# Performance work log

Hardware: AMD Instinct MI355X
Metric: run time of the kernel (lower is better)

Reference implementation:

```python
import jax, jax.numpy as jnp
import numpy as np

K_UP = 5
UP = 2
KS = 3
C_IN = 256


def pixel_shuffle(x, r):
    N, C, H, W = x.shape
    x = x.reshape(N, C // (r * r), r, r, H, W)
    return x.transpose(0, 1, 4, 2, 5, 3).reshape(N, C // (r * r), H * r, W * r)


def conv2d(x, w, b, pad):
    y = jax.lax.conv_general_dilated(
        x, w, window_strides=(1, 1), padding=[(pad, pad), (pad, pad)],
        dimension_numbers=('NCHW', 'OIHW', 'NCHW'))
    return y + b[None, :, None, None]


def setup_inputs() -> dict:
    key = jax.random.key(0)
    ks = jax.random.split(key, 7)
    C = C_IN
    Cd = C // 2
    Ce = UP * UP * K_UP * K_UP  # 100
    x = jax.random.normal(ks[0], (4, C, 64, 64), dtype=jnp.float32)
    # kaiming-normal-ish inits, biases small uniform (torch default)
    w_down = jax.random.normal(ks[1], (Cd, C, 1, 1), dtype=jnp.float32) * np.sqrt(2.0 / C)
    b_down = jax.random.uniform(ks[2], (Cd,), dtype=jnp.float32, minval=-0.05, maxval=0.05)
    w_enc = jax.random.normal(ks[3], (Ce, Cd, KS, KS), dtype=jnp.float32) * np.sqrt(2.0 / (Cd * KS * KS))
    b_enc = jax.random.uniform(ks[4], (Ce,), dtype=jnp.float32, minval=-0.05, maxval=0.05)
    w_out = jax.random.normal(ks[5], (C, C, 1, 1), dtype=jnp.float32) * np.sqrt(2.0 / C)
    b_out = jax.random.uniform(ks[6], (C,), dtype=jnp.float32, minval=-0.05, maxval=0.05)
    return {"x": x, "w_down": w_down, "b_down": b_down, "w_enc": w_enc,
            "b_enc": b_enc, "w_out": w_out, "b_out": b_out}


def reference(x, w_down, b_down, w_enc, b_enc, w_out, b_out):
    N, C, H, W = x.shape
    k2 = K_UP * K_UP  # 25
    u2 = UP * UP      # 4
    # kernel prediction branch
    kt = conv2d(x, w_down, b_down, 0)
    kt = conv2d(kt, w_enc, b_enc, KS // 2)
    kt = pixel_shuffle(kt, UP)              # (N, 25, H*UP, W*UP)
    kt = jax.nn.softmax(kt, axis=1)
    # unfold(2,UP,UP).unfold(3,UP,UP) -> (N,25,H,W,UP,UP) -> (N,H,W,25,UP*UP)
    kt = kt.reshape(N, k2, H, UP, W, UP).transpose(0, 2, 4, 1, 3, 5)
    kt = kt.reshape(N, H, W, k2, u2)
    # feature patches: pad then gather k_up x k_up window per pixel
    pad = K_UP // 2
    xp = jnp.pad(x, ((0, 0), (0, 0), (pad, pad), (pad, pad)))
    patches = jnp.stack(
        [xp[:, :, i:i + H, j:j + W] for i in range(K_UP) for j in range(K_UP)],
        axis=-1)                            # (N, C, H, W, 25)
    # per-pixel weighted sum: (N,H,W,C,25) @ (N,H,W,25,u2)
    out = jnp.einsum('nchwk,nhwkp->nchwp', patches, kt)  # (N,C,H,W,u2)
    out = out.transpose(0, 1, 4, 2, 3).reshape(N, C * u2, H, W)
    out = pixel_shuffle(out, UP)            # (N, C, H*UP, W*UP)
    return conv2d(out, w_out, b_out, 0)
```

## Files before the change

kernel.cpp:

```cpp
#include <hip/hip_runtime.h>
#include <hip/hip_bf16.h>


#define NB    4
#define NPIX  4096

typedef short s16x8 __attribute__((ext_vector_type(8)));
typedef float f32x4 __attribute__((ext_vector_type(4)));

#define MFMA16(a, b, c) __builtin_amdgcn_mfma_f32_16x16x32_bf16((a), (b), (c), 0, 0, 0)

__device__ __forceinline__ ushort f2b(float f) {
    __hip_bfloat16 h = __float2bfloat16(f);
    return *(ushort*)&h;
}
__device__ __forceinline__ float b2f(ushort u) {
    unsigned v = ((unsigned)u) << 16;
    return *(float*)&v;
}

__global__ __launch_bounds__(256) void prep_kernel(
    const float* __restrict__ wd, const float* __restrict__ wo,
    const float* __restrict__ we,
    ushort* __restrict__ wcomb, ushort* __restrict__ wrb)
{
    int idx = blockIdx.x * 256 + threadIdx.x;
    if (idx < 98304) {
        float v = (idx < 32768) ? wd[idx] : wo[idx - 32768];
        wcomb[idx] = f2b(v);
    } else if (idx < 227328) {
        int i = idx - 98304;
        int co = i / 1152, k = i - co * 1152;
        int tap = k >> 7, c = k & 127;
        float v = (co < 100) ? we[(co * 128 + c) * 9 + tap] : 0.0f;
        wrb[i] = f2b(v);
    }
}

__global__ __launch_bounds__(256, 2) void dual_gemm_kernel(
    const float*  __restrict__ X,
    const ushort* __restrict__ Wcomb,
    const float*  __restrict__ b_down,
    ushort* __restrict__ T1t,
    ushort* __restrict__ XOt)
{
    __shared__ __attribute__((aligned(16))) ushort xs[32][264];
    const int n = blockIdx.y, p0 = blockIdx.x * 32;
    const int tid = threadIdx.x, lane = tid & 63, wid = tid >> 6;
    const int l15 = lane & 15, l4 = lane >> 4;

    {
        const float* src = X + (size_t)n * 256 * NPIX + (size_t)tid * NPIX + p0;
        #pragma unroll
        for (int j = 0; j < 8; j++) {
            float4 v = *(const float4*)&src[j * 4];
            xs[j * 4 + 0][tid] = f2b(v.x);
            xs[j * 4 + 1][tid] = f2b(v.y);
            xs[j * 4 + 2][tid] = f2b(v.z);
            xs[j * 4 + 3][tid] = f2b(v.w);
        }
    }
    __syncthreads();

    const int wp = wid & 1;
    const int wc = wid >> 1;
    const int crow = wc * 192;

    f32x4 acc[12] = {};
    #pragma unroll 2
    for (int ks = 0; ks < 8; ks++) {
        int k0 = ks * 32 + l4 * 8;
        s16x8 a = *(const s16x8*)&xs[wp * 16 + l15][k0];
        #pragma unroll
        for (int cf = 0; cf < 12; cf++) {
            s16x8 b = *(const s16x8*)&Wcomb[(size_t)(crow + cf * 16 + l15) * 256 + k0];
            acc[cf] = MFMA16(a, b, acc[cf]);
        }
    }

    #pragma unroll
    for (int cf = 0; cf < 12; cf++) {
        int cbase = crow + cf * 16;
        int c = cbase + l15;
        if (cbase < 128) {
            float bb = b_down[c];
            #pragma unroll
            for (int r = 0; r < 4; r++) {
                int pix = p0 + wp * 16 + l4 * 4 + r;
                T1t[(size_t)(n * NPIX + pix) * 128 + c] = f2b(acc[cf][r] + bb);
            }
        } else {
            int c2 = c - 128;
            #pragma unroll
            for (int r = 0; r < 4; r++) {
                int pix = p0 + wp * 16 + l4 * 4 + r;
                XOt[(size_t)(n * NPIX + pix) * 256 + c2] = f2b(acc[cf][r]);
            }
        }
    }
}

__global__ __launch_bounds__(256, 3) void conv_sm_kernel(
    const ushort* __restrict__ T1t,
    const ushort* __restrict__ Wr,
    const float*  __restrict__ Benc,
    float* __restrict__ SMg)
{
    __shared__ __attribute__((aligned(16))) ushort hs[100][136];
    __shared__ float eld[64][101];

    const int n = blockIdx.y, tile = blockIdx.x;
    const int h0 = (tile >> 3) * 8, w0 = (tile & 7) * 8;
    const int tid = threadIdx.x, lane = tid & 63, wid = tid >> 6;
    const int l15 = lane & 15, l4 = lane >> 4;

    for (int u = tid; u < 1600; u += 256) {
        int hp = u >> 4, ch = u & 15;
        int r = hp / 10, s = hp - r * 10;
        int gh = h0 - 1 + r, gw = w0 - 1 + s;
        s16x8 v = {};
        if ((unsigned)gh < 64u && (unsigned)gw < 64u)
            v = *(const s16x8*)&T1t[((size_t)n * NPIX + gh * 64 + gw) * 128 + ch * 8];
        *(s16x8*)&hs[hp][ch * 8] = v;
    }
    __syncthreads();

    {
        const int pl = wid * 16 + l15;
        const int ph = pl >> 3, pw = pl & 7;
        f32x4 acc[7] = {};
        for (int tap = 0; tap < 9; tap++) {
            int dy = tap / 3, dx = tap - dy * 3;
            int hp = (ph + dy) * 10 + pw + dx;
            const ushort* hrow = &hs[hp][l4 * 8];
            const ushort* wrow = &Wr[(size_t)l15 * 1152 + tap * 128 + l4 * 8];
            #pragma unroll
            for (int cb = 0; cb < 4; cb++) {
                s16x8 b = *(const s16x8*)&hrow[cb * 32];
                #pragma unroll
                for (int mf = 0; mf < 7; mf++) {
                    s16x8 a = *(const s16x8*)&wrow[(size_t)mf * 16 * 1152 + cb * 32];
                    acc[mf] = MFMA16(a, b, acc[mf]);
                }
            }
        }
        #pragma unroll
        for (int mf = 0; mf < 7; mf++) {
            #pragma unroll
            for (int r = 0; r < 4; r++) {
                int co = mf * 16 + l4 * 4 + r;
                if (co < 100) eld[pl][co] = acc[mf][r] + Benc[co];
            }
        }
    }
    __syncthreads();

    {
        int p = tid & 3, pix = tid >> 2;
        float v[25];
        float mx = -1e30f;
        #pragma unroll
        for (int k = 0; k < 25; k++) { v[k] = eld[pix][4 * k + p]; mx = fmaxf(mx, v[k]); }
        float ssum = 0.0f;
        #pragma unroll
        for (int k = 0; k < 25; k++) { v[k] = __expf(v[k] - mx); ssum += v[k]; }
        float inv = 1.0f / ssum;
        float* dst = SMg + (size_t)(n * 64 + tile) * 6400;
        #pragma unroll
        for (int k = 0; k < 25; k++)
            dst[k * 256 + tid] = v[k] * inv;
    }
}

__global__ __launch_bounds__(256, 2) void reassembly_kernel(
    const float*  __restrict__ SMg,
    const ushort* __restrict__ XOt,
    const float*  __restrict__ Bout,
    float* __restrict__ Z)
{
    __shared__ __attribute__((aligned(16))) float sml[6400];
    __shared__ float xs[64][145];

    const int tile = blockIdx.x, oc = blockIdx.y, n = blockIdx.z;
    const int h0 = (tile >> 3) * 8, w0 = (tile & 7) * 8;
    const int tid = threadIdx.x;

    {
        const float* src = SMg + (size_t)(n * 64 + tile) * 6400;
        #pragma unroll
        for (int j = 0; j < 25; j++)
            sml[j * 256 + tid] = src[j * 256 + tid];
    }

    for (int u = tid; u < 2304; u += 256) {
        int hp = u >> 4, cg = u & 15;
        int r = hp / 12, s = hp - r * 12;
        int gh = h0 - 2 + r, gw = w0 - 2 + s;
        float v0 = 0.f, v1 = 0.f, v2 = 0.f, v3 = 0.f;
        if ((unsigned)gh < 64u && (unsigned)gw < 64u) {
            ushort4 raw = *(const ushort4*)&XOt[((size_t)n * NPIX + gh * 64 + gw) * 256 + oc * 64 + cg * 4];
            v0 = b2f(raw.x); v1 = b2f(raw.y); v2 = b2f(raw.z); v3 = b2f(raw.w);
        }
        xs[cg * 4 + 0][hp] = v0;
        xs[cg * 4 + 1][hp] = v1;
        xs[cg * 4 + 2][hp] = v2;
        xs[cg * 4 + 3][hp] = v3;
    }
    __syncthreads();

    const int pix = tid & 63;
    const int og = tid >> 6;
    const int ph = pix >> 3, pw = pix & 7;

    float acc[16][4] = {};
    for (int k = 0; k < 25; k++) {
        int di = k / 5, dj = k - di * 5;
        float4 wv = *(const float4*)&sml[k * 256 + pix * 4];
        int base = (ph + di) * 12 + pw + dj;
        #pragma unroll
        for (int i = 0; i < 16; i++) {
            float xv = xs[og * 16 + i][base];
            acc[i][0] += xv * wv.x;
            acc[i][1] += xv * wv.y;
            acc[i][2] += xv * wv.z;
            acc[i][3] += xv * wv.w;
        }
    }

    const int gh = h0 + ph, gw = w0 + pw;
    #pragma unroll
    for (int i = 0; i < 16; i++) {
        int o = oc * 64 + og * 16 + i;
        float bb = Bout[o];
        float2 r0 = make_float2(acc[i][0] + bb, acc[i][1] + bb);
        float2 r1 = make_float2(acc[i][2] + bb, acc[i][3] + bb);
        size_t zb = (((size_t)n * 256 + o) * 128 + 2 * gh) * 128 + 2 * gw;
        *(float2*)&Z[zb]       = r0;
        *(float2*)&Z[zb + 128] = r1;
    }
}

extern "C" void kernel_launch(void* const* d_in, const int* in_sizes, int n_in,
                              void* d_out, int out_size, void* d_ws, size_t ws_size,
                              hipStream_t stream) {
    const float* x      = (const float*)d_in[0];
    const float* w_down = (const float*)d_in[1];
    const float* b_down = (const float*)d_in[2];
    const float* w_enc  = (const float*)d_in[3];
    const float* b_enc  = (const float*)d_in[4];
    const float* w_out  = (const float*)d_in[5];
    const float* b_out  = (const float*)d_in[6];
    float* z = (float*)d_out;

    ushort* t1T   = (ushort*)d_ws;
    ushort* xoT   = t1T + 2097152;
    ushort* wcomb = xoT + 4194304;
    ushort* wrb   = wcomb + 98304;
    float*  smg   = (float*)(wrb + 129024);

    prep_kernel<<<888, 256, 0, stream>>>(w_down, w_out, w_enc, wcomb, wrb);
    dual_gemm_kernel<<<dim3(128, NB), 256, 0, stream>>>(x, wcomb, b_down, t1T, xoT);
    conv_sm_kernel<<<dim3(64, NB), 256, 0, stream>>>(t1T, wrb, b_enc, smg);
    reassembly_kernel<<<dim3(64, 4, NB), 256, 0, stream>>>(smg, xoT, b_out, z);
}
```

Before: 175.9 us.

## Rework dual-GEMM staging loads and reassembly thread mapping for wider accesses

In the dual GEMM kernel, the X tile staging now has each thread load two adjacent channels and write packed ushort2 values into shared memory, in place of per-element scattered stores. In the reassembly kernel, softmax weights are stored pixel-major in shared memory. Each thread now computes two horizontally adjacent pixels for 8 output channels instead of one pixel for 16 channels, which allows float4 output stores. The aim is to cut LDS bank conflicts and widen global writes, at the cost of a different register and LDS access pattern.

```diff
diff --git a/kernel.cpp b/kernel.cpp
--- a/kernel.cpp
+++ b/kernel.cpp
@@ -50,14 +50,23 @@
     const int l15 = lane & 15, l4 = lane >> 4;
 
     {
-        const float* src = X + (size_t)n * 256 * NPIX + (size_t)tid * NPIX + p0;
-        #pragma unroll
-        for (int j = 0; j < 8; j++) {
-            float4 v = *(const float4*)&src[j * 4];
-            xs[j * 4 + 0][tid] = f2b(v.x);
-            xs[j * 4 + 1][tid] = f2b(v.y);
-            xs[j * 4 + 2][tid] = f2b(v.z);
-            xs[j * 4 + 3][tid] = f2b(v.w);
+        const int pix4  = tid & 7;
+        const int cpair = tid >> 3;
+        const float* base = X + (size_t)n * 256 * NPIX + p0 + pix4 * 4;
+        #pragma unroll
+        for (int pp = 0; pp < 4; pp++) {
+            int c = pp * 64 + cpair * 2;
+            float4 va = *(const float4*)&base[(size_t)c * NPIX];
+            float4 vb = *(const float4*)&base[(size_t)(c + 1) * NPIX];
+            float va_[4] = {va.x, va.y, va.z, va.w};
+            float vb_[4] = {vb.x, vb.y, vb.z, vb.w};
+            #pragma unroll
+            for (int j = 0; j < 4; j++) {
+                ushort2 w;
+                w.x = f2b(va_[j]);
+                w.y = f2b(vb_[j]);
+                *(ushort2*)&xs[pix4 * 4 + j][c] = w;
+            }
         }
     }
     __syncthreads();
@@ -178,7 +187,7 @@
     const float*  __restrict__ Bout,
     float* __restrict__ Z)
 {
-    __shared__ __attribute__((aligned(16))) float sml[6400];
+    __shared__ __attribute__((aligned(16))) float sml[64][100];
     __shared__ float xs[64][145];
 
     const int tile = blockIdx.x, oc = blockIdx.y, n = blockIdx.z;
@@ -187,9 +196,10 @@
 
     {
         const float* src = SMg + (size_t)(n * 64 + tile) * 6400;
+        int pix = tid >> 2, p = tid & 3;
         #pragma unroll
         for (int j = 0; j < 25; j++)
-            sml[j * 256 + tid] = src[j * 256 + tid];
+            sml[pix][j * 4 + p] = src[j * 256 + tid];
     }
 
     for (int u = tid; u < 2304; u += 256) {
@@ -208,35 +218,42 @@
     }
     __syncthreads();
 
-    const int pix = tid & 63;
-    const int og = tid >> 6;
-    const int ph = pix >> 3, pw = pix & 7;
-
-    float acc[16][4] = {};
+    const int pw2 = tid & 3;
+    const int ph  = (tid >> 2) & 7;
+    const int og  = tid >> 5;
+    const int pix0 = ph * 8 + pw2 * 2;
+
+    float acc[8][8] = {};
     for (int k = 0; k < 25; k++) {
         int di = k / 5, dj = k - di * 5;
-        float4 wv = *(const float4*)&sml[k * 256 + pix * 4];
-        int base = (ph + di) * 12 + pw + dj;
-        #pragma unroll
-        for (int i = 0; i < 16; i++) {
-            float xv = xs[og * 16 + i][base];
-            acc[i][0] += xv * wv.x;
-            acc[i][1] += xv * wv.y;
-            acc[i][2] += xv * wv.z;
-            acc[i][3] += xv * wv.w;
-        }
-    }
-
-    const int gh = h0 + ph, gw = w0 + pw;
+        float4 wv0 = *(const float4*)&sml[pix0][k * 4];
+        float4 wv1 = *(const float4*)&sml[pix0 + 1][k * 4];
+        int base = (ph + di) * 12 + pw2 * 2 + dj;
+        #pragma unroll
+        for (int i = 0; i < 8; i++) {
+            float xv0 = xs[og * 8 + i][base];
+            float xv1 = xs[og * 8 + i][base + 1];
+            acc[i][0] += xv0 * wv0.x;
+            acc[i][1] += xv0 * wv0.y;
+            acc[i][2] += xv0 * wv0.z;
+            acc[i][3] += xv0 * wv0.w;
+            acc[i][4] += xv1 * wv1.x;
+            acc[i][5] += xv1 * wv1.y;
+            acc[i][6] += xv1 * wv1.z;
+            acc[i][7] += xv1 * wv1.w;
+        }
+    }
+
+    const int gh = h0 + ph;
     #pragma unroll
-    for (int i = 0; i < 16; i++) {
-        int o = oc * 64 + og * 16 + i;
+    for (int i = 0; i < 8; i++) {
+        int o = oc * 64 + og * 8 + i;
         float bb = Bout[o];
-        float2 r0 = make_float2(acc[i][0] + bb, acc[i][1] + bb);
-        float2 r1 = make_float2(acc[i][2] + bb, acc[i][3] + bb);
-        size_t zb = (((size_t)n * 256 + o) * 128 + 2 * gh) * 128 + 2 * gw;
-        *(float2*)&Z[zb]       = r0;
-        *(float2*)&Z[zb + 128] = r1;
+        float4 v0 = make_float4(acc[i][0] + bb, acc[i][1] + bb, acc[i][4] + bb, acc[i][5] + bb);
+        float4 v1 = make_float4(acc[i][2] + bb, acc[i][3] + bb, acc[i][6] + bb, acc[i][7] + bb);
+        size_t zb = (((size_t)n * 256 + o) * 128 + 2 * gh) * 128 + 2 * w0 + 4 * pw2;
+        *(float4*)&Z[zb]       = v0;
+        *(float4*)&Z[zb + 128] = v1;
     }
 }
 
```

Result: no change. 174.2 us (-1.0%).
